# Optimization experiments

Hardware: AMD Instinct MI355X
Metric: run time of the kernel (lower is better)

The kernel has to match this reference:

```python
import jax, jax.numpy as jnp
import numpy as np

D_MODEL = 2048
NUM_HEADS = 16
HEAD_DIM = D_MODEL // NUM_HEADS  # 128
B, L = 2, 2048


def setup_inputs() -> dict:
    key = jax.random.key(0)
    ks = jax.random.split(key, 7)
    s = 0.02
    return {
        "x": jax.random.normal(ks[0], (B, L, D_MODEL), dtype=jnp.float32),
        "Wq_w": jax.random.normal(ks[1], (D_MODEL, D_MODEL), dtype=jnp.float32) * s,
        "Wq_b": jnp.zeros((D_MODEL,), dtype=jnp.float32),
        "Wk_w": jax.random.normal(ks[2], (HEAD_DIM, D_MODEL), dtype=jnp.float32) * s,
        "Wk_b": jnp.zeros((HEAD_DIM,), dtype=jnp.float32),
        "Wv_w": jax.random.normal(ks[3], (HEAD_DIM, D_MODEL), dtype=jnp.float32) * s,
        "Wv_b": jnp.zeros((HEAD_DIM,), dtype=jnp.float32),
    }


def reference(x, Wq_w, Wq_b, Wk_w, Wk_b, Wv_w, Wv_b):
    b, l, _ = x.shape
    # torch Linear: y = x @ W.T + b
    Q = (x @ Wq_w.T + Wq_b).reshape(b, l, NUM_HEADS, HEAD_DIM)  # [B,L,H,D]
    K = x @ Wk_w.T + Wk_b  # [B,L,D] single shared KV head (MQA)
    V = x @ Wv_w.T + Wv_b  # [B,L,D]
    scale = 1.0 / jnp.sqrt(jnp.float32(HEAD_DIM))
    # scores: [B,H,Lq,Lk]; K's head dim (size 1 in torch) broadcasts -> contract over d only
    scores = jnp.einsum("bqhd,bkd->bhqk", Q, K) * scale
    attn = jax.nn.softmax(scores, axis=-1)
    out = jnp.einsum("bhqk,bkd->bqhd", attn, V)  # [B,L,H,D]
    return out.reshape(b, l, D_MODEL)
```

## Files before the change

kernel.cpp:

```cpp
#include <hip/hip_runtime.h>
#include <hip/hip_bf16.h>


typedef unsigned short u16;
typedef unsigned int u32;
typedef __bf16 bf16x8 __attribute__((ext_vector_type(8)));
typedef float f32x16 __attribute__((ext_vector_type(16)));
typedef u16 u16x4 __attribute__((ext_vector_type(4)));
typedef u32 u32x4 __attribute__((ext_vector_type(4)));

#define MFMA32(a, b, c) __builtin_amdgcn_mfma_f32_32x32x16_bf16((a), (b), (c), 0, 0, 0)

__device__ __forceinline__ u16 f2bf(float f) {
  __hip_bfloat16 h = __float2bfloat16(f);
  return __builtin_bit_cast(u16, h);
}

__device__ __forceinline__ float fexp2(float x) {
#if __has_builtin(__builtin_amdgcn_exp2f)
  return __builtin_amdgcn_exp2f(x);
#else
  return exp2f(x);
#endif
}

__device__ __forceinline__ void cp16(const void* g, void* l) {
  __builtin_amdgcn_global_load_lds(
      (const __attribute__((address_space(1))) u32*)g,
      (__attribute__((address_space(3))) u32*)l, 16, 0, 0);
}

__device__ __forceinline__ f32x16 zero16() {
  f32x16 v;
#pragma unroll
  for (int i = 0; i < 16; ++i) v[i] = 0.f;
  return v;
}

__global__ __launch_bounds__(256) void k_convert(
    const float* __restrict__ x, const float* __restrict__ wq,
    const float* __restrict__ wk, const float* __restrict__ wv,
    u16* __restrict__ xb, u16* __restrict__ wqb,
    u16* __restrict__ wkb, u16* __restrict__ wvb) {
  int idx = blockIdx.x * 256 + threadIdx.x;
  for (int i = idx; i < 3276800; i += 524288) {
    float4 v; u16* dst;
    if (i < 2097152) {
      v = ((const float4*)x)[i]; dst = xb + (size_t)i * 4;
    } else if (i < 3145728) {
      int j = i - 2097152; v = ((const float4*)wq)[j]; dst = wqb + (size_t)j * 4;
    } else if (i < 3211264) {
      int j = i - 3145728; v = ((const float4*)wk)[j]; dst = wkb + (size_t)j * 4;
    } else {
      int j = i - 3211264; v = ((const float4*)wv)[j]; dst = wvb + (size_t)j * 4;
    }
    u16x4 o;
    o[0] = f2bf(v.x); o[1] = f2bf(v.y); o[2] = f2bf(v.z); o[3] = f2bf(v.w);
    *(u16x4*)dst = o;
  }
}

__global__ __launch_bounds__(256) void k_gemm_qkv(
    const u16* __restrict__ xb, const u16* __restrict__ wqb,
    const u16* __restrict__ wkb, const u16* __restrict__ wvb,
    const float* __restrict__ bq, const float* __restrict__ bk, const float* __restrict__ bv,
    u16* __restrict__ qout, u16* __restrict__ kout, u16* __restrict__ vtout) {
  __shared__ __align__(16) u16 sh[10240];
  const int tid = threadIdx.x;
  const int w = tid >> 6, lane = tid & 63, ln = lane & 31, hi = lane >> 5;
  const int wr = w >> 1, wc = w & 1;
  const int m0 = blockIdx.x * 128;
  const int by = blockIdx.y;
  const int mode = (by < 16) ? 0 : (by - 15);
  const int n0loc = (mode == 0) ? by * 128 : 0;
  const u16* __restrict__ Bp = (mode == 0) ? wqb : (mode == 1 ? wkb : wvb);
  const u16* Arow = xb + (size_t)m0 * 2048;
  const u16* Brow = Bp + (size_t)n0loc * 2048;

  const u16* sb[5];
#pragma unroll
  for (int i = 0; i < 5; ++i) {
    int s = (w + i * 4) * 64 + lane;
    const u16* base; int r, c;
    if (s < 640) { r = s / 5; c = s % 5; if (c > 3) c = 0; base = Arow; }
    else { int s2 = s - 640; r = s2 / 5; c = s2 % 5; if (c > 3) c = 0; base = Brow; }
    sb[i] = base + (size_t)r * 2048 + c * 8;
  }

  f32x16 acc[2][2];
  acc[0][0] = zero16(); acc[0][1] = zero16(); acc[1][0] = zero16(); acc[1][1] = zero16();

  const int a0off = (wr * 64 + ln) * 40 + hi * 8;
  const int b0off = 5120 + (wc * 64 + ln) * 40 + hi * 8;

  for (int k0 = 0; k0 < 2048; k0 += 32) {
    __syncthreads();
#pragma unroll
    for (int i = 0; i < 5; ++i)
      cp16(sb[i] + k0, (void*)(sh + (w + i * 4) * 512));
    __syncthreads();
#pragma unroll
    for (int kc = 0; kc < 2; ++kc) {
      const int ko = kc * 16;
      bf16x8 a0 = *(const bf16x8*)&sh[a0off + ko];
      bf16x8 a1 = *(const bf16x8*)&sh[a0off + 1280 + ko];
      bf16x8 b0 = *(const bf16x8*)&sh[b0off + ko];
      bf16x8 b1 = *(const bf16x8*)&sh[b0off + 1280 + ko];
      acc[0][0] = MFMA32(a0, b0, acc[0][0]);
      acc[0][1] = MFMA32(a0, b1, acc[0][1]);
      acc[1][0] = MFMA32(a1, b0, acc[1][0]);
      acc[1][1] = MFMA32(a1, b1, acc[1][1]);
    }
  }

  const float qscale = 0.12751744630098356f;
#pragma unroll
  for (int fm = 0; fm < 2; ++fm) {
#pragma unroll
    for (int fn = 0; fn < 2; ++fn) {
      f32x16 a = acc[fm][fn];
      const int mbase = m0 + wr * 64 + fm * 32;
      const int nloc = n0loc + wc * 64 + fn * 32 + ln;
      if (mode == 0) {
        const float bsc = bq[nloc] * qscale;
#pragma unroll
        for (int r = 0; r < 16; ++r) {
          int row = (r & 3) + 8 * (r >> 2) + 4 * hi;
          qout[(size_t)(mbase + row) * 2048 + nloc] = f2bf(a[r] * qscale + bsc);
        }
      } else if (mode == 1) {
        const float bb = bk[nloc];
#pragma unroll
        for (int r = 0; r < 16; ++r) {
          int row = (r & 3) + 8 * (r >> 2) + 4 * hi;
          kout[(size_t)(mbase + row) * 128 + nloc] = f2bf(a[r] + bb);
        }
      } else {
        const float bb = bv[nloc];
#pragma unroll
        for (int r = 0; r < 16; ++r) {
          int row = (r & 3) + 8 * (r >> 2) + 4 * hi;
          int m = mbase + row;
          vtout[(size_t)((m >> 11) * 128 + nloc) * 2048 + (m & 2047)] = f2bf(a[r] + bb);
        }
      }
    }
  }
}

__global__ __launch_bounds__(256, 1) void k_attn(
    const u16* __restrict__ qb, const u16* __restrict__ kb, const u16* __restrict__ vtb,
    float* __restrict__ out) {
  __shared__ __align__(16) u16 sh[35840];
  const int tid = threadIdx.x;
  const int w = tid >> 6, lane = tid & 63, ln = lane & 31, hi = lane >> 5;
  const int q0 = blockIdx.x * 256, h = blockIdx.y, b = blockIdx.z;
  const size_t bL = (size_t)b * 2048;
  const u16* kbase = kb + bL * 128;
  const u16* vbase = vtb + (size_t)b * 128 * 2048;

  bf16x8 qfA[8], qfB[8];
  {
    const u16* qrowA = qb + (bL + q0 + w * 64 + ln) * 2048 + h * 128 + hi * 8;
    const u16* qrowB = qrowA + 32 * 2048;
#pragma unroll
    for (int kc = 0; kc < 8; ++kc) {
      qfA[kc] = *(const bf16x8*)(qrowA + kc * 16);
      qfB[kc] = *(const bf16x8*)(qrowB + kc * 16);
    }
  }

  const u16* sb[9]; int smul[9];
  const int nsl = (38 - w) >> 2;
#pragma unroll
  for (int i = 0; i < 9; ++i) {
    int sl = w + i * 4;
    if (sl < 35) {
      int s = sl * 64 + lane;
      if (s < 1088) {
        int r = s / 17, c = s % 17; if (c > 15) c = 0;
        sb[i] = kbase + r * 128 + c * 8; smul[i] = 128;
      } else {
        int s2 = s - 1088; int r = s2 / 9, c = s2 % 9; if (c > 7) c = 0;
        sb[i] = vbase + (size_t)r * 2048 + c * 8; smul[i] = 1;
      }
    } else { sb[i] = kbase; smul[i] = 0; }
  }

#pragma unroll
  for (int i = 0; i < 9; ++i)
    if (i < nsl) cp16(sb[i], (void*)(sh + (w + i * 4) * 512));
  __syncthreads();

  f32x16 oA[4], oB[4];
#pragma unroll
  for (int dg = 0; dg < 4; ++dg) { oA[dg] = zero16(); oB[dg] = zero16(); }
  float lA = 0.f, lB = 0.f;

  const int kro = ln * 136 + hi * 8;
  const int vro = 8704 + ln * 72 + hi * 8;

  for (int it = 0; it < 32; ++it) {
    const int cur = (it & 1) * 17920;
    const int nxt = 17920 - cur;
    const size_t k0n = (it < 31) ? (size_t)(it + 1) * 64 : 0;
#pragma unroll
    for (int i = 0; i < 9; ++i)
      if (i < nsl) cp16(sb[i] + k0n * smul[i], (void*)(sh + nxt + (w + i * 4) * 512));

    f32x16 s0A = zero16(), s1A = zero16(), s0B = zero16(), s1B = zero16();
#pragma unroll
    for (int kc = 0; kc < 8; ++kc) {
      bf16x8 a0 = *(const bf16x8*)&sh[cur + kro + kc * 16];
      bf16x8 a1 = *(const bf16x8*)&sh[cur + kro + 32 * 136 + kc * 16];
      s0A = MFMA32(a0, qfA[kc], s0A);
      s1A = MFMA32(a1, qfA[kc], s1A);
      s0B = MFMA32(a0, qfB[kc], s0B);
      s1B = MFMA32(a1, qfB[kc], s1B);
    }

    u32 pkA[16], pkB[16];
#pragma unroll
    for (int i = 0; i < 8; ++i) {
      float a = fexp2(s0A[2 * i]), c = fexp2(s0A[2 * i + 1]);
      pkA[i] = __builtin_amdgcn_perm(__builtin_bit_cast(u32, c),
                                     __builtin_bit_cast(u32, a), 0x07060302u);
      float d = fexp2(s1A[2 * i]), e = fexp2(s1A[2 * i + 1]);
      pkA[8 + i] = __builtin_amdgcn_perm(__builtin_bit_cast(u32, e),
                                         __builtin_bit_cast(u32, d), 0x07060302u);
      float f = fexp2(s0B[2 * i]), g = fexp2(s0B[2 * i + 1]);
      pkB[i] = __builtin_amdgcn_perm(__builtin_bit_cast(u32, g),
                                     __builtin_bit_cast(u32, f), 0x07060302u);
      float p = fexp2(s1B[2 * i]), q = fexp2(s1B[2 * i + 1]);
      pkB[8 + i] = __builtin_amdgcn_perm(__builtin_bit_cast(u32, q),
                                         __builtin_bit_cast(u32, p), 0x07060302u);
    }
#pragma unroll
    for (int i = 0; i < 16; ++i) {
      lA += __builtin_bit_cast(float, pkA[i] << 16);
      lA += __builtin_bit_cast(float, pkA[i] & 0xffff0000u);
      lB += __builtin_bit_cast(float, pkB[i] << 16);
      lB += __builtin_bit_cast(float, pkB[i] & 0xffff0000u);
    }

    bf16x8 pfA[4], pfB[4];
#pragma unroll
    for (int c = 0; c < 4; ++c) {
      const int wb = 4 * c;
#pragma unroll
      for (int sel = 0; sel < 2; ++sel) {
        const u32* mat = sel ? pkB : pkA;
        u32 send0 = hi ? mat[wb] : mat[wb + 2];
        u32 send1 = hi ? mat[wb + 1] : mat[wb + 3];
        u32 r0 = (u32)__shfl_xor((int)send0, 32, 64);
        u32 r1 = (u32)__shfl_xor((int)send1, 32, 64);
        u32x4 v;
        v[0] = hi ? r0 : mat[wb];
        v[1] = hi ? r1 : mat[wb + 1];
        v[2] = hi ? mat[wb + 2] : r0;
        v[3] = hi ? mat[wb + 3] : r1;
        if (sel) pfB[c] = __builtin_bit_cast(bf16x8, v);
        else     pfA[c] = __builtin_bit_cast(bf16x8, v);
      }
    }

#pragma unroll
    for (int c = 0; c < 4; ++c)
#pragma unroll
      for (int dg = 0; dg < 4; ++dg) {
        bf16x8 va = *(const bf16x8*)&sh[cur + vro + dg * 2304 + c * 16];
        oA[dg] = MFMA32(va, pfA[c], oA[dg]);
        oB[dg] = MFMA32(va, pfB[c], oB[dg]);
      }

    __syncthreads();
  }

  lA += __shfl_xor(lA, 32, 64);
  lB += __shfl_xor(lB, 32, 64);
  const float invA = 1.0f / lA, invB = 1.0f / lB;

  float* orowA = out + (bL + q0 + w * 64 + ln) * 2048 + h * 128 + hi * 4;
  float* orowB = orowA + 32 * 2048;
#pragma unroll
  for (int dg = 0; dg < 4; ++dg)
#pragma unroll
    for (int rq = 0; rq < 4; ++rq) {
      float4 va, vb;
      va.x = oA[dg][rq * 4 + 0] * invA; va.y = oA[dg][rq * 4 + 1] * invA;
      va.z = oA[dg][rq * 4 + 2] * invA; va.w = oA[dg][rq * 4 + 3] * invA;
      vb.x = oB[dg][rq * 4 + 0] * invB; vb.y = oB[dg][rq * 4 + 1] * invB;
      vb.z = oB[dg][rq * 4 + 2] * invB; vb.w = oB[dg][rq * 4 + 3] * invB;
      *(float4*)&orowA[dg * 32 + rq * 8] = va;
      *(float4*)&orowB[dg * 32 + rq * 8] = vb;
    }
}

extern "C" void kernel_launch(void* const* d_in, const int* in_sizes, int n_in,
                              void* d_out, int out_size, void* d_ws, size_t ws_size,
                              hipStream_t stream) {
  const float* x  = (const float*)d_in[0];
  const float* wq = (const float*)d_in[1];
  const float* bq = (const float*)d_in[2];
  const float* wk = (const float*)d_in[3];
  const float* bk = (const float*)d_in[4];
  const float* wv = (const float*)d_in[5];
  const float* bv = (const float*)d_in[6];
  float* out = (float*)d_out;
  char* ws = (char*)d_ws;

  u16* xb   = (u16*)(ws);
  u16* wqb  = (u16*)(ws + 16777216);
  u16* wkb  = (u16*)(ws + 25165824);
  u16* wvb  = (u16*)(ws + 25690112);
  u16* qb   = (u16*)(ws + 26214400);
  u16* kbuf = (u16*)(ws + 42991616);
  u16* vtb  = (u16*)(ws + 44040192);

  k_convert<<<2048, 256, 0, stream>>>(x, wq, wk, wv, xb, wqb, wkb, wvb);
  k_gemm_qkv<<<dim3(32, 18), 256, 0, stream>>>(xb, wqb, wkb, wvb, bq, bk, bv, qb, kbuf, vtb);
  k_attn<<<dim3(8, 16, 2), 256, 0, stream>>>(qb, kbuf, vtb, out);
}
```

Measured before the change: 275.8 us.

## Split attention work across 8 waves with one 32-row query tile each

```diff
diff --git a/kernel.cpp b/kernel.cpp
--- a/kernel.cpp
+++ b/kernel.cpp
@@ -148,7 +148,7 @@
   }
 }
 
-__global__ __launch_bounds__(256, 1) void k_attn(
+__global__ __launch_bounds__(512, 2) void k_attn(
     const u16* __restrict__ qb, const u16* __restrict__ kb, const u16* __restrict__ vtb,
     float* __restrict__ out) {
   __shared__ __align__(16) u16 sh[35840];
@@ -159,22 +159,18 @@
   const u16* kbase = kb + bL * 128;
   const u16* vbase = vtb + (size_t)b * 128 * 2048;
 
-  bf16x8 qfA[8], qfB[8];
+  bf16x8 qf[8];
   {
-    const u16* qrowA = qb + (bL + q0 + w * 64 + ln) * 2048 + h * 128 + hi * 8;
-    const u16* qrowB = qrowA + 32 * 2048;
-#pragma unroll
-    for (int kc = 0; kc < 8; ++kc) {
-      qfA[kc] = *(const bf16x8*)(qrowA + kc * 16);
-      qfB[kc] = *(const bf16x8*)(qrowB + kc * 16);
-    }
-  }
-
-  const u16* sb[9]; int smul[9];
-  const int nsl = (38 - w) >> 2;
-#pragma unroll
-  for (int i = 0; i < 9; ++i) {
-    int sl = w + i * 4;
+    const u16* qrow = qb + (bL + q0 + w * 32 + ln) * 2048 + h * 128 + hi * 8;
+#pragma unroll
+    for (int kc = 0; kc < 8; ++kc) qf[kc] = *(const bf16x8*)(qrow + kc * 16);
+  }
+
+  const u16* sb[5]; int smul[5];
+  const int nsl = (w < 3) ? 5 : 4;
+#pragma unroll
+  for (int i = 0; i < 5; ++i) {
+    int sl = w + i * 8;
     if (sl < 35) {
       int s = sl * 64 + lane;
       if (s < 1088) {
@@ -188,14 +184,14 @@
   }
 
 #pragma unroll
-  for (int i = 0; i < 9; ++i)
-    if (i < nsl) cp16(sb[i], (void*)(sh + (w + i * 4) * 512));
+  for (int i = 0; i < 5; ++i)
+    if (i < nsl) cp16(sb[i], (void*)(sh + (w + i * 8) * 512));
   __syncthreads();
 
-  f32x16 oA[4], oB[4];
-#pragma unroll
-  for (int dg = 0; dg < 4; ++dg) { oA[dg] = zero16(); oB[dg] = zero16(); }
-  float lA = 0.f, lB = 0.f;
+  f32x16 o[4];
+#pragma unroll
+  for (int dg = 0; dg < 4; ++dg) o[dg] = zero16();
+  float l = 0.f;
 
   const int kro = ln * 136 + hi * 8;
   const int vro = 8704 + ln * 72 + hi * 8;
@@ -205,63 +201,48 @@
     const int nxt = 17920 - cur;
     const size_t k0n = (it < 31) ? (size_t)(it + 1) * 64 : 0;
 #pragma unroll
-    for (int i = 0; i < 9; ++i)
-      if (i < nsl) cp16(sb[i] + k0n * smul[i], (void*)(sh + nxt + (w + i * 4) * 512));
-
-    f32x16 s0A = zero16(), s1A = zero16(), s0B = zero16(), s1B = zero16();
+    for (int i = 0; i < 5; ++i)
+      if (i < nsl) cp16(sb[i] + k0n * smul[i], (void*)(sh + nxt + (w + i * 8) * 512));
+
+    f32x16 s0 = zero16(), s1 = zero16();
 #pragma unroll
     for (int kc = 0; kc < 8; ++kc) {
       bf16x8 a0 = *(const bf16x8*)&sh[cur + kro + kc * 16];
       bf16x8 a1 = *(const bf16x8*)&sh[cur + kro + 32 * 136 + kc * 16];
-      s0A = MFMA32(a0, qfA[kc], s0A);
-      s1A = MFMA32(a1, qfA[kc], s1A);
-      s0B = MFMA32(a0, qfB[kc], s0B);
-      s1B = MFMA32(a1, qfB[kc], s1B);
-    }
-
-    u32 pkA[16], pkB[16];
+      s0 = MFMA32(a0, qf[kc], s0);
+      s1 = MFMA32(a1, qf[kc], s1);
+    }
+
+    u32 pk[16];
 #pragma unroll
     for (int i = 0; i < 8; ++i) {
-      float a = fexp2(s0A[2 * i]), c = fexp2(s0A[2 * i + 1]);
-      pkA[i] = __builtin_amdgcn_perm(__builtin_bit_cast(u32, c),
-                                     __builtin_bit_cast(u32, a), 0x07060302u);
-      float d = fexp2(s1A[2 * i]), e = fexp2(s1A[2 * i + 1]);
-      pkA[8 + i] = __builtin_amdgcn_perm(__builtin_bit_cast(u32, e),
-                                         __builtin_bit_cast(u32, d), 0x07060302u);
-      float f = fexp2(s0B[2 * i]), g = fexp2(s0B[2 * i + 1]);
-      pkB[i] = __builtin_amdgcn_perm(__builtin_bit_cast(u32, g),
-                                     __builtin_bit_cast(u32, f), 0x07060302u);
-      float p = fexp2(s1B[2 * i]), q = fexp2(s1B[2 * i + 1]);
-      pkB[8 + i] = __builtin_amdgcn_perm(__builtin_bit_cast(u32, q),
-                                         __builtin_bit_cast(u32, p), 0x07060302u);
+      float a = fexp2(s0[2 * i]), c = fexp2(s0[2 * i + 1]);
+      pk[i] = __builtin_amdgcn_perm(__builtin_bit_cast(u32, c),
+                                    __builtin_bit_cast(u32, a), 0x07060302u);
+      float d = fexp2(s1[2 * i]), e = fexp2(s1[2 * i + 1]);
+      pk[8 + i] = __builtin_amdgcn_perm(__builtin_bit_cast(u32, e),
+                                        __builtin_bit_cast(u32, d), 0x07060302u);
     }
 #pragma unroll
     for (int i = 0; i < 16; ++i) {
-      lA += __builtin_bit_cast(float, pkA[i] << 16);
-      lA += __builtin_bit_cast(float, pkA[i] & 0xffff0000u);
-      lB += __builtin_bit_cast(float, pkB[i] << 16);
-      lB += __builtin_bit_cast(float, pkB[i] & 0xffff0000u);
-    }
-
-    bf16x8 pfA[4], pfB[4];
+      l += __builtin_bit_cast(float, pk[i] << 16);
+      l += __builtin_bit_cast(float, pk[i] & 0xffff0000u);
+    }
+
+    bf16x8 pf[4];
 #pragma unroll
     for (int c = 0; c < 4; ++c) {
       const int wb = 4 * c;
-#pragma unroll
-      for (int sel = 0; sel < 2; ++sel) {
-        const u32* mat = sel ? pkB : pkA;
-        u32 send0 = hi ? mat[wb] : mat[wb + 2];
-        u32 send1 = hi ? mat[wb + 1] : mat[wb + 3];
-        u32 r0 = (u32)__shfl_xor((int)send0, 32, 64);
-        u32 r1 = (u32)__shfl_xor((int)send1, 32, 64);
-        u32x4 v;
-        v[0] = hi ? r0 : mat[wb];
-        v[1] = hi ? r1 : mat[wb + 1];
-        v[2] = hi ? mat[wb + 2] : r0;
-        v[3] = hi ? mat[wb + 3] : r1;
-        if (sel) pfB[c] = __builtin_bit_cast(bf16x8, v);
-        else     pfA[c] = __builtin_bit_cast(bf16x8, v);
-      }
+      u32 send0 = hi ? pk[wb] : pk[wb + 2];
+      u32 send1 = hi ? pk[wb + 1] : pk[wb + 3];
+      u32 r0 = (u32)__shfl_xor((int)send0, 32, 64);
+      u32 r1 = (u32)__shfl_xor((int)send1, 32, 64);
+      u32x4 v;
+      v[0] = hi ? r0 : pk[wb];
+      v[1] = hi ? r1 : pk[wb + 1];
+      v[2] = hi ? pk[wb + 2] : r0;
+      v[3] = hi ? pk[wb + 3] : r1;
+      pf[c] = __builtin_bit_cast(bf16x8, v);
     }
 
 #pragma unroll
@@ -269,30 +250,24 @@
 #pragma unroll
       for (int dg = 0; dg < 4; ++dg) {
         bf16x8 va = *(const bf16x8*)&sh[cur + vro + dg * 2304 + c * 16];
-        oA[dg] = MFMA32(va, pfA[c], oA[dg]);
-        oB[dg] = MFMA32(va, pfB[c], oB[dg]);
+        o[dg] = MFMA32(va, pf[c], o[dg]);
       }
 
     __syncthreads();
   }
 
-  lA += __shfl_xor(lA, 32, 64);
-  lB += __shfl_xor(lB, 32, 64);
-  const float invA = 1.0f / lA, invB = 1.0f / lB;
-
-  float* orowA = out + (bL + q0 + w * 64 + ln) * 2048 + h * 128 + hi * 4;
-  float* orowB = orowA + 32 * 2048;
+  l += __shfl_xor(l, 32, 64);
+  const float inv = 1.0f / l;
+
+  float* orow = out + (bL + q0 + w * 32 + ln) * 2048 + h * 128 + hi * 4;
 #pragma unroll
   for (int dg = 0; dg < 4; ++dg)
 #pragma unroll
     for (int rq = 0; rq < 4; ++rq) {
-      float4 va, vb;
-      va.x = oA[dg][rq * 4 + 0] * invA; va.y = oA[dg][rq * 4 + 1] * invA;
-      va.z = oA[dg][rq * 4 + 2] * invA; va.w = oA[dg][rq * 4 + 3] * invA;
-      vb.x = oB[dg][rq * 4 + 0] * invB; vb.y = oB[dg][rq * 4 + 1] * invB;
-      vb.z = oB[dg][rq * 4 + 2] * invB; vb.w = oB[dg][rq * 4 + 3] * invB;
-      *(float4*)&orowA[dg * 32 + rq * 8] = va;
-      *(float4*)&orowB[dg * 32 + rq * 8] = vb;
+      float4 v4;
+      v4.x = o[dg][rq * 4 + 0] * inv; v4.y = o[dg][rq * 4 + 1] * inv;
+      v4.z = o[dg][rq * 4 + 2] * inv; v4.w = o[dg][rq * 4 + 3] * inv;
+      *(float4*)&orow[dg * 32 + rq * 8] = v4;
     }
 }
 
@@ -319,5 +294,5 @@
 
   k_convert<<<2048, 256, 0, stream>>>(x, wq, wk, wv, xb, wqb, wkb, wvb);
   k_gemm_qkv<<<dim3(32, 18), 256, 0, stream>>>(xb, wqb, wkb, wvb, bq, bk, bv, qb, kbuf, vtb);
-  k_attn<<<dim3(8, 16, 2), 256, 0, stream>>>(qb, kbuf, vtb, out);
-}
+  k_attn<<<dim3(8, 16, 2), 512, 0, stream>>>(qb, kbuf, vtb, out);
+}
```

New measurement: 248.1 us. 1.11x faster.
